# Kernel tuning notes

Hardware: AMD Instinct MI355X
Metric: run time of the kernel (lower is better)

## Reference

```python
import jax, jax.numpy as jnp
import numpy as np

T = 256          # tokens
H = 1024         # hidden_size
E = 64           # num_experts
I = 512          # routed intermediate_size
SI = 2048        # shared_expert_intermediate_size
TOP_K = 6
N_GROUP = 8
TOPK_GROUP = 4
ROUTED_SCALE = 2.5


def setup_inputs() -> dict:
    key = jax.random.key(0)
    ks = jax.random.split(key, 9)
    s = 0.02
    return {
        "hidden_states": jax.random.normal(ks[0], (T, H), jnp.float32),
        "gate_w": jax.random.normal(ks[1], (E, H), jnp.float32) * s,
        "e_bias": jax.random.normal(ks[2], (E,), jnp.float32) * 0.01,
        "w1": jax.random.normal(ks[3], (E, I, H), jnp.float32) * s,  # gate proj
        "w3": jax.random.normal(ks[4], (E, I, H), jnp.float32) * s,  # up proj
        "w2": jax.random.normal(ks[5], (E, H, I), jnp.float32) * s,  # down proj
        "ws_gate": jax.random.normal(ks[6], (SI, H), jnp.float32) * s,
        "ws_up": jax.random.normal(ks[7], (SI, H), jnp.float32) * s,
        "ws_down": jax.random.normal(ks[8], (H, SI), jnp.float32) * s,
    }


def _noaux_tc_routing(logits, e_bias):
    # DeepSeek-V3 group-limited sigmoid routing (is_thop=False path).
    scores = jax.nn.sigmoid(logits)                         # [T, E]
    swb = scores + e_bias                                   # bias only picks experts
    t, e = scores.shape
    g = swb.reshape(t, N_GROUP, e // N_GROUP)
    group_scores = jax.lax.top_k(g, 2)[0].sum(-1)           # top-2 sum per group [T, G]
    _, gidx = jax.lax.top_k(group_scores, TOPK_GROUP)
    gmask = jax.nn.one_hot(gidx, N_GROUP, dtype=scores.dtype).sum(-2)  # [T, G]
    smask = jnp.repeat(gmask, e // N_GROUP, axis=-1)        # [T, E]
    _, tidx = jax.lax.top_k(swb * smask, TOP_K)
    nmask = jax.nn.one_hot(tidx, e, dtype=scores.dtype).sum(-2)
    s = scores * nmask
    s = s / (s.sum(-1, keepdims=True) + 1e-20) * ROUTED_SCALE  # [T, E], TOP_K nonzeros
    # torch code returns topk(values, indices) of s; s itself is the dense
    # combine-weight matrix with exactly those values scattered at the indices.
    return s


def reference(hidden_states, gate_w, e_bias, w1, w3, w2, ws_gate, ws_up, ws_down):
    x = hidden_states
    # gate: cublas_mm with fp32 output
    logits = (x @ gate_w.T).astype(jnp.float32)             # [T, E]
    cw = _noaux_tc_routing(logits, e_bias)                  # [T, E] combine weights

    # routed experts: gated MLP per expert, combined by routing weights
    h1 = jnp.einsum('th,eih->tei', x, w1)
    h3 = jnp.einsum('th,eih->tei', x, w3)
    act = jax.nn.silu(h1) * h3                              # [T, E, I]
    eo = jnp.einsum('tei,ehi->teh', act, w2)                # [T, E, H]
    routed = jnp.einsum('teh,te->th', eo, cw.astype(x.dtype))

    # shared experts: GatedMLP
    shared = (jax.nn.silu(x @ ws_gate.T) * (x @ ws_up.T)) @ ws_down.T

    return shared + routed
```

## Files before the change

kernel.cpp:

```cpp
#include <hip/hip_runtime.h>
#include <math.h>

#define T_TOK 256
#define H_DIM 1024
#define E_NUM 64
#define I_DIM 512
#define SI_DIM 2048

#define BN 64
#define BM 32
#define BK 64
#define LDB 72

typedef __attribute__((ext_vector_type(8))) short short8;
typedef __attribute__((ext_vector_type(8))) __bf16 bf16x8;
typedef __attribute__((ext_vector_type(4))) float floatx4;
typedef __attribute__((ext_vector_type(4))) unsigned short ushort4v;

static __device__ __forceinline__ unsigned short f2bf(float f) {
  unsigned u = __float_as_uint(f);
  u += 0x7FFFu + ((u >> 16) & 1u);
  return (unsigned short)(u >> 16);
}

static __device__ __forceinline__ ushort4v pack4(floatx4 v) {
  ushort4v b;
  b[0] = f2bf(v[0]); b[1] = f2bf(v[1]); b[2] = f2bf(v[2]); b[3] = f2bf(v[3]);
  return b;
}

static __device__ __forceinline__ floatx4 mfma16(bf16x8 a, bf16x8 b, floatx4 c) {
  return __builtin_amdgcn_mfma_f32_16x16x32_bf16(a, b, c, 0, 0, 0);
}

__global__ __launch_bounds__(256) void gate_route_kernel(
    const float* __restrict__ x, const float* __restrict__ gw,
    const float* __restrict__ ebias, unsigned short* __restrict__ xbf,
    int* __restrict__ cnt, int* __restrict__ tok_list,
    float* __restrict__ wt_list) {
  const int t = blockIdx.x;
  const int j = threadIdx.x;
  __shared__ float xs[H_DIM];
  __shared__ double pd[4 * 64];

  floatx4 v = ((const floatx4*)(x + (size_t)t * H_DIM))[j];
  xs[4 * j + 0] = v[0]; xs[4 * j + 1] = v[1];
  xs[4 * j + 2] = v[2]; xs[4 * j + 3] = v[3];
  ((ushort4v*)(xbf + (size_t)t * H_DIM))[j] = pack4(v);
  __syncthreads();

  const int e = j & 63, ch = j >> 6;
  const float* wr = gw + (size_t)e * H_DIM + ch * 256;
  const float* xc = xs + ch * 256;
  double acc = 0.0;
  for (int i = 0; i < 64; ++i) {
    floatx4 w = ((const floatx4*)wr)[i];
    acc += (double)xc[4 * i + 0] * (double)w[0]
         + (double)xc[4 * i + 1] * (double)w[1]
         + (double)xc[4 * i + 2] * (double)w[2]
         + (double)xc[4 * i + 3] * (double)w[3];
  }
  pd[ch * 64 + e] = acc;
  __syncthreads();

  if (j < 64) {
    const int lane = j;
    const double logit = pd[lane] + pd[64 + lane] + pd[128 + lane] + pd[192 + lane];
    const double score = 1.0 / (1.0 + exp(-logit));
    const double swb = score + (double)ebias[lane];

    double m1 = swb, m2 = -1.0e300;
    #pragma unroll
    for (int d = 1; d < 8; d <<= 1) {
      double o1 = __shfl_xor(m1, d);
      double o2 = __shfl_xor(m2, d);
      double hi = fmax(m1, o1), lo = fmin(m1, o1);
      m1 = hi;
      m2 = fmax(lo, fmax(m2, o2));
    }
    const double gscore = m1 + m2;

    double gs[8];
    #pragma unroll
    for (int g = 0; g < 8; ++g) gs[g] = __shfl(gscore, g << 3);
    unsigned gsel = 0;
    #pragma unroll
    for (int it = 0; it < 4; ++it) {
      int best = 0; double bv = -1.0e300;
      #pragma unroll
      for (int g = 0; g < 8; ++g) {
        bool taken = (gsel >> g) & 1u;
        if (!taken && gs[g] > bv) { bv = gs[g]; best = g; }
      }
      gsel |= 1u << best;
    }

    double key = ((gsel >> (lane >> 3)) & 1u) ? swb : -1.0e300;
    int selected = 0;
    for (int it = 0; it < 6; ++it) {
      double vv = key; int idx = lane;
      #pragma unroll
      for (int d = 1; d < 64; d <<= 1) {
        double ov = __shfl_xor(vv, d);
        int oi = __shfl_xor(idx, d);
        if (ov > vv || (ov == vv && oi < idx)) { vv = ov; idx = oi; }
      }
      if (lane == idx) { selected = 1; key = -1.0e300; }
    }

    double ssum = selected ? score : 0.0;
    #pragma unroll
    for (int d = 1; d < 64; d <<= 1) ssum += __shfl_xor(ssum, d);

    if (selected) {
      float wgt = (float)(score / (ssum + 1e-20) * 2.5);
      int p = atomicAdd(&cnt[lane], 1);
      tok_list[lane * T_TOK + p] = t;
      wt_list[lane * T_TOK + p] = wgt;
    }
  }
}

__global__ __launch_bounds__(256, 2) void routed_gu_kernel(
    const unsigned short* __restrict__ xbf, const float* __restrict__ w1,
    const float* __restrict__ w3, const int* __restrict__ cnt,
    const int* __restrict__ tok_list, unsigned short* __restrict__ act_r) {
  __shared__ unsigned short sBg[BN * LDB];
  __shared__ unsigned short sBu[BN * LDB];
  __shared__ unsigned short sA[BM * LDB];
  __shared__ int stok[BM];

  const int e = blockIdx.x >> 3;
  const int n0 = (blockIdx.x & 7) * BN;
  const int j = threadIdx.x;
  const int wv = j >> 6, lane = j & 63;
  const int q = lane >> 4, c = lane & 15;
  const int ne = cnt[e];
  const int* tl = tok_list + e * T_TOK;
  unsigned short* ap = act_r + (size_t)e * T_TOK * I_DIM;
  const float* wgB = w1 + ((size_t)e * I_DIM + n0) * H_DIM;
  const float* wuB = w3 + ((size_t)e * I_DIM + n0) * H_DIM;

  const int wrow = j >> 4;
  const int wcol = (j & 15) * 4;
  const int arow = j >> 3;
  const int acol = (j & 7) * 8;

  for (int m0 = 0; m0 < ne; m0 += BM) {
    __syncthreads();
    if (j < BM) {
      int r = m0 + j;
      stok[j] = (r < ne) ? tl[r] : 0;
    }
    __syncthreads();
    const unsigned short* aRow = xbf + (size_t)stok[arow] * H_DIM;

    floatx4 pg[4], pu[4];
    bf16x8 pa;
    #pragma unroll
    for (int p = 0; p < 4; ++p) {
      pg[p] = *(const floatx4*)(wgB + (size_t)(p * 16 + wrow) * H_DIM + wcol);
      pu[p] = *(const floatx4*)(wuB + (size_t)(p * 16 + wrow) * H_DIM + wcol);
    }
    pa = *(const bf16x8*)(aRow + acol);

    floatx4 ag0 = (floatx4)0.0f, ag1 = (floatx4)0.0f;
    floatx4 au0 = (floatx4)0.0f, au1 = (floatx4)0.0f;
    for (int k0 = 0; k0 < H_DIM; k0 += BK) {
      if (k0) __syncthreads();
      #pragma unroll
      for (int p = 0; p < 4; ++p) {
        *(ushort4v*)(sBg + (p * 16 + wrow) * LDB + wcol) = pack4(pg[p]);
        *(ushort4v*)(sBu + (p * 16 + wrow) * LDB + wcol) = pack4(pu[p]);
      }
      *(bf16x8*)(sA + arow * LDB + acol) = pa;
      __syncthreads();
      if (k0 + BK < H_DIM) {
        const int kn = k0 + BK;
        #pragma unroll
        for (int p = 0; p < 4; ++p) {
          pg[p] = *(const floatx4*)(wgB + (size_t)(p * 16 + wrow) * H_DIM + kn + wcol);
          pu[p] = *(const floatx4*)(wuB + (size_t)(p * 16 + wrow) * H_DIM + kn + wcol);
        }
        pa = *(const bf16x8*)(aRow + kn + acol);
      }
      #pragma unroll
      for (int kk = 0; kk < BK; kk += 32) {
        const int ko = kk + q * 8;
        bf16x8 bg = *(const bf16x8*)(sBg + (wv * 16 + c) * LDB + ko);
        bf16x8 bu = *(const bf16x8*)(sBu + (wv * 16 + c) * LDB + ko);
        bf16x8 a0 = *(const bf16x8*)(sA + c * LDB + ko);
        bf16x8 a1 = *(const bf16x8*)(sA + (16 + c) * LDB + ko);
        ag0 = mfma16(a0, bg, ag0);
        ag1 = mfma16(a1, bg, ag1);
        au0 = mfma16(a0, bu, au0);
        au1 = mfma16(a1, bu, au1);
      }
    }
    #pragma unroll
    for (int s = 0; s < 2; ++s) {
      floatx4 g = s ? ag1 : ag0;
      floatx4 u = s ? au1 : au0;
      #pragma unroll
      for (int r = 0; r < 4; ++r) {
        const int m = m0 + s * 16 + q * 4 + r;
        if (m < ne) {
          float gg = g[r], uu = u[r];
          float a = gg / (1.0f + __expf(-gg)) * uu;
          ap[(size_t)m * I_DIM + n0 + wv * 16 + c] = f2bf(a);
        }
      }
    }
  }
}

__global__ __launch_bounds__(256, 2) void shared_gu_kernel(
    const unsigned short* __restrict__ xbf, const float* __restrict__ wsg,
    const float* __restrict__ wsu, unsigned short* __restrict__ act_s) {
  __shared__ unsigned short sBg[BN * LDB];
  __shared__ unsigned short sBu[BN * LDB];
  __shared__ unsigned short sA[BM * LDB];

  const int n0 = (blockIdx.x & 31) * BN;
  const int m0 = (blockIdx.x >> 5) * BM;
  const int j = threadIdx.x;
  const int wv = j >> 6, lane = j & 63;
  const int q = lane >> 4, c = lane & 15;
  const float* wgB = wsg + (size_t)n0 * H_DIM;
  const float* wuB = wsu + (size_t)n0 * H_DIM;

  const int wrow = j >> 4, wcol = (j & 15) * 4;
  const int arow = j >> 3, acol = (j & 7) * 8;
  const unsigned short* aRow = xbf + (size_t)(m0 + arow) * H_DIM;

  floatx4 pg[4], pu[4];
  bf16x8 pa;
  #pragma unroll
  for (int p = 0; p < 4; ++p) {
    pg[p] = *(const floatx4*)(wgB + (size_t)(p * 16 + wrow) * H_DIM + wcol);
    pu[p] = *(const floatx4*)(wuB + (size_t)(p * 16 + wrow) * H_DIM + wcol);
  }
  pa = *(const bf16x8*)(aRow + acol);

  floatx4 ag0 = (floatx4)0.0f, ag1 = (floatx4)0.0f;
  floatx4 au0 = (floatx4)0.0f, au1 = (floatx4)0.0f;
  for (int k0 = 0; k0 < H_DIM; k0 += BK) {
    if (k0) __syncthreads();
    #pragma unroll
    for (int p = 0; p < 4; ++p) {
      *(ushort4v*)(sBg + (p * 16 + wrow) * LDB + wcol) = pack4(pg[p]);
      *(ushort4v*)(sBu + (p * 16 + wrow) * LDB + wcol) = pack4(pu[p]);
    }
    *(bf16x8*)(sA + arow * LDB + acol) = pa;
    __syncthreads();
    if (k0 + BK < H_DIM) {
      const int kn = k0 + BK;
      #pragma unroll
      for (int p = 0; p < 4; ++p) {
        pg[p] = *(const floatx4*)(wgB + (size_t)(p * 16 + wrow) * H_DIM + kn + wcol);
        pu[p] = *(const floatx4*)(wuB + (size_t)(p * 16 + wrow) * H_DIM + kn + wcol);
      }
      pa = *(const bf16x8*)(aRow + kn + acol);
    }
    #pragma unroll
    for (int kk = 0; kk < BK; kk += 32) {
      const int ko = kk + q * 8;
      bf16x8 bg = *(const bf16x8*)(sBg + (wv * 16 + c) * LDB + ko);
      bf16x8 bu = *(const bf16x8*)(sBu + (wv * 16 + c) * LDB + ko);
      bf16x8 a0 = *(const bf16x8*)(sA + c * LDB + ko);
      bf16x8 a1 = *(const bf16x8*)(sA + (16 + c) * LDB + ko);
      ag0 = mfma16(a0, bg, ag0);
      ag1 = mfma16(a1, bg, ag1);
      au0 = mfma16(a0, bu, au0);
      au1 = mfma16(a1, bu, au1);
    }
  }
  #pragma unroll
  for (int s = 0; s < 2; ++s) {
    floatx4 g = s ? ag1 : ag0;
    floatx4 u = s ? au1 : au0;
    #pragma unroll
    for (int r = 0; r < 4; ++r) {
      const int m = m0 + s * 16 + q * 4 + r;
      float gg = g[r], uu = u[r];
      float a = gg / (1.0f + __expf(-gg)) * uu;
      act_s[(size_t)m * SI_DIM + n0 + wv * 16 + c] = f2bf(a);
    }
  }
}

__global__ __launch_bounds__(256, 2) void shared_down_kernel(
    const unsigned short* __restrict__ act_s, const float* __restrict__ wsd,
    float* __restrict__ out) {
  __shared__ unsigned short sB[BN * LDB];
  __shared__ unsigned short sA[BM * LDB];

  const int n0 = (blockIdx.x & 15) * BN;
  const int m0 = ((blockIdx.x >> 4) & 7) * BM;
  const int kh = blockIdx.x >> 7;
  const int kbeg = kh * (SI_DIM / 2);
  const int j = threadIdx.x;
  const int wv = j >> 6, lane = j & 63;
  const int q = lane >> 4, c = lane & 15;
  const float* wB = wsd + (size_t)n0 * SI_DIM;

  const int wrow = j >> 4, wcol = (j & 15) * 4;
  const int arow = j >> 3, acol = (j & 7) * 8;
  const unsigned short* aRow = act_s + (size_t)(m0 + arow) * SI_DIM;

  floatx4 pw[4];
  bf16x8 pa;
  #pragma unroll
  for (int p = 0; p < 4; ++p) {
    pw[p] = *(const floatx4*)(wB + (size_t)(p * 16 + wrow) * SI_DIM + kbeg + wcol);
  }
  pa = *(const bf16x8*)(aRow + kbeg + acol);

  floatx4 ac0 = (floatx4)0.0f, ac1 = (floatx4)0.0f;
  for (int kr = 0; kr < SI_DIM / 2; kr += BK) {
    const int k0 = kbeg + kr;
    if (kr) __syncthreads();
    #pragma unroll
    for (int p = 0; p < 4; ++p) {
      *(ushort4v*)(sB + (p * 16 + wrow) * LDB + wcol) = pack4(pw[p]);
    }
    *(bf16x8*)(sA + arow * LDB + acol) = pa;
    __syncthreads();
    if (kr + BK < SI_DIM / 2) {
      const int kn = k0 + BK;
      #pragma unroll
      for (int p = 0; p < 4; ++p) {
        pw[p] = *(const floatx4*)(wB + (size_t)(p * 16 + wrow) * SI_DIM + kn + wcol);
      }
      pa = *(const bf16x8*)(aRow + kn + acol);
    }
    #pragma unroll
    for (int kk = 0; kk < BK; kk += 32) {
      const int ko = kk + q * 8;
      bf16x8 b = *(const bf16x8*)(sB + (wv * 16 + c) * LDB + ko);
      bf16x8 a0 = *(const bf16x8*)(sA + c * LDB + ko);
      bf16x8 a1 = *(const bf16x8*)(sA + (16 + c) * LDB + ko);
      ac0 = mfma16(a0, b, ac0);
      ac1 = mfma16(a1, b, ac1);
    }
  }
  #pragma unroll
  for (int s = 0; s < 2; ++s) {
    floatx4 d = s ? ac1 : ac0;
    #pragma unroll
    for (int r = 0; r < 4; ++r) {
      const int m = m0 + s * 16 + q * 4 + r;
      atomicAdd(&out[(size_t)m * H_DIM + n0 + wv * 16 + c], d[r]);
    }
  }
}

__global__ __launch_bounds__(256, 2) void routed_down_kernel(
    const unsigned short* __restrict__ act_r, const float* __restrict__ w2,
    const int* __restrict__ cnt, const int* __restrict__ tok_list,
    const float* __restrict__ wt_list, float* __restrict__ out) {
  __shared__ unsigned short sB[BN * LDB];
  __shared__ unsigned short sA[BM * LDB];
  __shared__ int stok[BM];
  __shared__ float swl[BM];

  const int e = blockIdx.x >> 4;
  const int n0 = (blockIdx.x & 15) * BN;
  const int j = threadIdx.x;
  const int wv = j >> 6, lane = j & 63;
  const int q = lane >> 4, c = lane & 15;
  const int ne = cnt[e];
  const int* tl = tok_list + e * T_TOK;
  const float* wl = wt_list + e * T_TOK;
  const unsigned short* apb = act_r + (size_t)e * T_TOK * I_DIM;
  const float* wB = w2 + ((size_t)e * H_DIM + n0) * I_DIM;

  const int wrow = j >> 4, wcol = (j & 15) * 4;
  const int arow = j >> 3, acol = (j & 7) * 8;

  for (int m0 = 0; m0 < ne; m0 += BM) {
    __syncthreads();
    if (j < BM) {
      int r = m0 + j;
      bool ok = r < ne;
      stok[j] = ok ? tl[r] : 0;
      swl[j] = ok ? wl[r] : 0.0f;
    }
    int ar = m0 + arow;
    if (ar >= T_TOK) ar = T_TOK - 1;
    const unsigned short* aRow = apb + (size_t)ar * I_DIM;

    floatx4 pw[4];
    bf16x8 pa;
    #pragma unroll
    for (int p = 0; p < 4; ++p) {
      pw[p] = *(const floatx4*)(wB + (size_t)(p * 16 + wrow) * I_DIM + wcol);
    }
    pa = *(const bf16x8*)(aRow + acol);

    floatx4 ac0 = (floatx4)0.0f, ac1 = (floatx4)0.0f;
    for (int k0 = 0; k0 < I_DIM; k0 += BK) {
      __syncthreads();
      #pragma unroll
      for (int p = 0; p < 4; ++p) {
        *(ushort4v*)(sB + (p * 16 + wrow) * LDB + wcol) = pack4(pw[p]);
      }
      *(bf16x8*)(sA + arow * LDB + acol) = pa;
      __syncthreads();
      if (k0 + BK < I_DIM) {
        const int kn = k0 + BK;
        #pragma unroll
        for (int p = 0; p < 4; ++p) {
          pw[p] = *(const floatx4*)(wB + (size_t)(p * 16 + wrow) * I_DIM + kn + wcol);
        }
        pa = *(const bf16x8*)(aRow + kn + acol);
      }
      #pragma unroll
      for (int kk = 0; kk < BK; kk += 32) {
        const int ko = kk + q * 8;
        bf16x8 b = *(const bf16x8*)(sB + (wv * 16 + c) * LDB + ko);
        bf16x8 a0 = *(const bf16x8*)(sA + c * LDB + ko);
        bf16x8 a1 = *(const bf16x8*)(sA + (16 + c) * LDB + ko);
        ac0 = mfma16(a0, b, ac0);
        ac1 = mfma16(a1, b, ac1);
      }
    }
    #pragma unroll
    for (int s = 0; s < 2; ++s) {
      floatx4 d = s ? ac1 : ac0;
      #pragma unroll
      for (int r = 0; r < 4; ++r) {
        const int mi = s * 16 + q * 4 + r;
        if (m0 + mi < ne) {
          atomicAdd(&out[(size_t)stok[mi] * H_DIM + n0 + wv * 16 + c],
                    d[r] * swl[mi]);
        }
      }
    }
  }
}

extern "C" void kernel_launch(void* const* d_in, const int* in_sizes, int n_in,
                              void* d_out, int out_size, void* d_ws, size_t ws_size,
                              hipStream_t stream) {
  const float* x   = (const float*)d_in[0];
  const float* gw  = (const float*)d_in[1];
  const float* eb  = (const float*)d_in[2];
  const float* w1  = (const float*)d_in[3];
  const float* w3  = (const float*)d_in[4];
  const float* w2  = (const float*)d_in[5];
  const float* wsg = (const float*)d_in[6];
  const float* wsu = (const float*)d_in[7];
  const float* wsd = (const float*)d_in[8];
  float* out = (float*)d_out;

  char* ws = (char*)d_ws;
  unsigned short* xbf   = (unsigned short*)(ws);
  unsigned short* act_s = (unsigned short*)(ws + 524288);
  int*   cnt            = (int*)(ws + 1572864);
  int*   tok            = (int*)(ws + 1573120);
  float* wt             = (float*)(ws + 1638656);
  unsigned short* act_r = (unsigned short*)(ws + 1704192);

  hipMemsetAsync(cnt, 0, E_NUM * sizeof(int), stream);
  hipMemsetAsync(out, 0, (size_t)T_TOK * H_DIM * sizeof(float), stream);
  gate_route_kernel<<<dim3(T_TOK), dim3(256), 0, stream>>>(x, gw, eb, xbf, cnt, tok, wt);
  routed_gu_kernel<<<dim3(E_NUM * (I_DIM / BN)), dim3(256), 0, stream>>>(xbf, w1, w3, cnt, tok, act_r);
  shared_gu_kernel<<<dim3((SI_DIM / BN) * (T_TOK / BM)), dim3(256), 0, stream>>>(xbf, wsg, wsu, act_s);
  shared_down_kernel<<<dim3((H_DIM / BN) * (T_TOK / BM) * 2), dim3(256), 0, stream>>>(act_s, wsd, out);
  routed_down_kernel<<<dim3(E_NUM * (H_DIM / BN)), dim3(256), 0, stream>>>(act_r, w2, cnt, tok, wt, out);
}
```

Measured before the change: 469.8 us.

## Load fp32 weights directly into MFMA operand registers, stage only activations in LDS

The four GEMM kernels stop staging the fp32 weight tiles through shared memory. Each lane now reads its own weight row straight from global memory, converts it to bf16 in registers and feeds it to the MFMA as the B operand, with a one-step register prefetch. Only the activation rows go to LDS, staged in large 512-wide chunks with an XOR swizzle to avoid bank conflicts, which cuts the number of barriers per K loop. The cost is less coalesced global weight loads, each lane striding across rows, and less latency hiding, since only one step is prefetched and there is no LDS double buffering.

```diff
diff --git a/kernel.cpp b/kernel.cpp
--- a/kernel.cpp
+++ b/kernel.cpp
@@ -9,13 +9,12 @@
 
 #define BN 64
 #define BM 32
-#define BK 64
-#define LDB 72
 
 typedef __attribute__((ext_vector_type(8))) short short8;
 typedef __attribute__((ext_vector_type(8))) __bf16 bf16x8;
 typedef __attribute__((ext_vector_type(4))) float floatx4;
 typedef __attribute__((ext_vector_type(4))) unsigned short ushort4v;
+typedef __attribute__((ext_vector_type(8))) unsigned short ushort8;
 
 static __device__ __forceinline__ unsigned short f2bf(float f) {
   unsigned u = __float_as_uint(f);
@@ -27,6 +26,14 @@
   ushort4v b;
   b[0] = f2bf(v[0]); b[1] = f2bf(v[1]); b[2] = f2bf(v[2]); b[3] = f2bf(v[3]);
   return b;
+}
+
+static __device__ __forceinline__ bf16x8 pack8(floatx4 a, floatx4 b) {
+  ushort8 s;
+  s[0] = f2bf(a[0]); s[1] = f2bf(a[1]); s[2] = f2bf(a[2]); s[3] = f2bf(a[3]);
+  s[4] = f2bf(b[0]); s[5] = f2bf(b[1]); s[6] = f2bf(b[2]); s[7] = f2bf(b[3]);
+  union { ushort8 u; bf16x8 v; } cv; cv.u = s;
+  return cv.v;
 }
 
 static __device__ __forceinline__ floatx4 mfma16(bf16x8 a, bf16x8 b, floatx4 c) {
@@ -125,72 +132,61 @@
     const unsigned short* __restrict__ xbf, const float* __restrict__ w1,
     const float* __restrict__ w3, const int* __restrict__ cnt,
     const int* __restrict__ tok_list, unsigned short* __restrict__ act_r) {
-  __shared__ unsigned short sBg[BN * LDB];
-  __shared__ unsigned short sBu[BN * LDB];
-  __shared__ unsigned short sA[BM * LDB];
-  __shared__ int stok[BM];
+  __shared__ __align__(16) char sAB[BM * 1024];
 
   const int e = blockIdx.x >> 3;
   const int n0 = (blockIdx.x & 7) * BN;
   const int j = threadIdx.x;
   const int wv = j >> 6, lane = j & 63;
   const int q = lane >> 4, c = lane & 15;
+  const int kq = q * 8;
   const int ne = cnt[e];
+  if (ne <= 0) return;
   const int* tl = tok_list + e * T_TOK;
   unsigned short* ap = act_r + (size_t)e * T_TOK * I_DIM;
-  const float* wgB = w1 + ((size_t)e * I_DIM + n0) * H_DIM;
-  const float* wuB = w3 + ((size_t)e * I_DIM + n0) * H_DIM;
-
-  const int wrow = j >> 4;
-  const int wcol = (j & 15) * 4;
-  const int arow = j >> 3;
-  const int acol = (j & 7) * 8;
+
+  const float* wgR = w1 + ((size_t)e * I_DIM + n0 + wv * 16 + c) * H_DIM;
+  const float* wuR = w3 + ((size_t)e * I_DIM + n0 + wv * 16 + c) * H_DIM;
+
+  const int sr = j >> 3, st8 = (j & 7) * 8;
+  const int xrs = (sr & 7) << 4;
+  const int xr0 = (c & 7) << 4;
 
   for (int m0 = 0; m0 < ne; m0 += BM) {
-    __syncthreads();
-    if (j < BM) {
-      int r = m0 + j;
-      stok[j] = (r < ne) ? tl[r] : 0;
-    }
-    __syncthreads();
-    const unsigned short* aRow = xbf + (size_t)stok[arow] * H_DIM;
-
-    floatx4 pg[4], pu[4];
-    bf16x8 pa;
-    #pragma unroll
-    for (int p = 0; p < 4; ++p) {
-      pg[p] = *(const floatx4*)(wgB + (size_t)(p * 16 + wrow) * H_DIM + wcol);
-      pu[p] = *(const floatx4*)(wuB + (size_t)(p * 16 + wrow) * H_DIM + wcol);
-    }
-    pa = *(const bf16x8*)(aRow + acol);
+    const int tok = (m0 + sr < ne) ? tl[m0 + sr] : tl[m0];
+    const unsigned short* aRow = xbf + (size_t)tok * H_DIM;
+
+    floatx4 cg0 = *(const floatx4*)(wgR + kq);
+    floatx4 cg1 = *(const floatx4*)(wgR + kq + 4);
+    floatx4 cu0 = *(const floatx4*)(wuR + kq);
+    floatx4 cu1 = *(const floatx4*)(wuR + kq + 4);
 
     floatx4 ag0 = (floatx4)0.0f, ag1 = (floatx4)0.0f;
     floatx4 au0 = (floatx4)0.0f, au1 = (floatx4)0.0f;
-    for (int k0 = 0; k0 < H_DIM; k0 += BK) {
-      if (k0) __syncthreads();
-      #pragma unroll
-      for (int p = 0; p < 4; ++p) {
-        *(ushort4v*)(sBg + (p * 16 + wrow) * LDB + wcol) = pack4(pg[p]);
-        *(ushort4v*)(sBu + (p * 16 + wrow) * LDB + wcol) = pack4(pu[p]);
-      }
-      *(bf16x8*)(sA + arow * LDB + acol) = pa;
+
+    for (int half = 0; half < 2; ++half) {
+      const int kbase = half * 512;
       __syncthreads();
-      if (k0 + BK < H_DIM) {
-        const int kn = k0 + BK;
-        #pragma unroll
-        for (int p = 0; p < 4; ++p) {
-          pg[p] = *(const floatx4*)(wgB + (size_t)(p * 16 + wrow) * H_DIM + kn + wcol);
-          pu[p] = *(const floatx4*)(wuB + (size_t)(p * 16 + wrow) * H_DIM + kn + wcol);
+      #pragma unroll
+      for (int i = 0; i < 512; i += 64) {
+        const int col = st8 + i;
+        *(bf16x8*)(sAB + sr * 1024 + ((2 * col) ^ xrs)) =
+            *(const bf16x8*)(aRow + kbase + col);
+      }
+      __syncthreads();
+      for (int kcl = 0; kcl < 512; kcl += 32) {
+        const int kc = kbase + kcl;
+        bf16x8 bg = pack8(cg0, cg1);
+        bf16x8 bu = pack8(cu0, cu1);
+        if (kc + 32 < H_DIM) {
+          cg0 = *(const floatx4*)(wgR + kc + 32 + kq);
+          cg1 = *(const floatx4*)(wgR + kc + 32 + kq + 4);
+          cu0 = *(const floatx4*)(wuR + kc + 32 + kq);
+          cu1 = *(const floatx4*)(wuR + kc + 32 + kq + 4);
         }
-        pa = *(const bf16x8*)(aRow + kn + acol);
-      }
-      #pragma unroll
-      for (int kk = 0; kk < BK; kk += 32) {
-        const int ko = kk + q * 8;
-        bf16x8 bg = *(const bf16x8*)(sBg + (wv * 16 + c) * LDB + ko);
-        bf16x8 bu = *(const bf16x8*)(sBu + (wv * 16 + c) * LDB + ko);
-        bf16x8 a0 = *(const bf16x8*)(sA + c * LDB + ko);
-        bf16x8 a1 = *(const bf16x8*)(sA + (16 + c) * LDB + ko);
+        const int kb = 2 * (kcl + kq);
+        bf16x8 a0 = *(const bf16x8*)(sAB + c * 1024 + (kb ^ xr0));
+        bf16x8 a1 = *(const bf16x8*)(sAB + (16 + c) * 1024 + (kb ^ xr0));
         ag0 = mfma16(a0, bg, ag0);
         ag1 = mfma16(a1, bg, ag1);
         au0 = mfma16(a0, bu, au0);
@@ -217,58 +213,54 @@
 __global__ __launch_bounds__(256, 2) void shared_gu_kernel(
     const unsigned short* __restrict__ xbf, const float* __restrict__ wsg,
     const float* __restrict__ wsu, unsigned short* __restrict__ act_s) {
-  __shared__ unsigned short sBg[BN * LDB];
-  __shared__ unsigned short sBu[BN * LDB];
-  __shared__ unsigned short sA[BM * LDB];
+  __shared__ __align__(16) char sAB[BM * 1024];
 
   const int n0 = (blockIdx.x & 31) * BN;
   const int m0 = (blockIdx.x >> 5) * BM;
   const int j = threadIdx.x;
   const int wv = j >> 6, lane = j & 63;
   const int q = lane >> 4, c = lane & 15;
-  const float* wgB = wsg + (size_t)n0 * H_DIM;
-  const float* wuB = wsu + (size_t)n0 * H_DIM;
-
-  const int wrow = j >> 4, wcol = (j & 15) * 4;
-  const int arow = j >> 3, acol = (j & 7) * 8;
-  const unsigned short* aRow = xbf + (size_t)(m0 + arow) * H_DIM;
-
-  floatx4 pg[4], pu[4];
-  bf16x8 pa;
-  #pragma unroll
-  for (int p = 0; p < 4; ++p) {
-    pg[p] = *(const floatx4*)(wgB + (size_t)(p * 16 + wrow) * H_DIM + wcol);
-    pu[p] = *(const floatx4*)(wuB + (size_t)(p * 16 + wrow) * H_DIM + wcol);
-  }
-  pa = *(const bf16x8*)(aRow + acol);
+  const int kq = q * 8;
+
+  const float* wgR = wsg + (size_t)(n0 + wv * 16 + c) * H_DIM;
+  const float* wuR = wsu + (size_t)(n0 + wv * 16 + c) * H_DIM;
+
+  const int sr = j >> 3, st8 = (j & 7) * 8;
+  const int xrs = (sr & 7) << 4;
+  const int xr0 = (c & 7) << 4;
+  const unsigned short* aRow = xbf + (size_t)(m0 + sr) * H_DIM;
+
+  floatx4 cg0 = *(const floatx4*)(wgR + kq);
+  floatx4 cg1 = *(const floatx4*)(wgR + kq + 4);
+  floatx4 cu0 = *(const floatx4*)(wuR + kq);
+  floatx4 cu1 = *(const floatx4*)(wuR + kq + 4);
 
   floatx4 ag0 = (floatx4)0.0f, ag1 = (floatx4)0.0f;
   floatx4 au0 = (floatx4)0.0f, au1 = (floatx4)0.0f;
-  for (int k0 = 0; k0 < H_DIM; k0 += BK) {
-    if (k0) __syncthreads();
-    #pragma unroll
-    for (int p = 0; p < 4; ++p) {
-      *(ushort4v*)(sBg + (p * 16 + wrow) * LDB + wcol) = pack4(pg[p]);
-      *(ushort4v*)(sBu + (p * 16 + wrow) * LDB + wcol) = pack4(pu[p]);
-    }
-    *(bf16x8*)(sA + arow * LDB + acol) = pa;
-    __syncthreads();
-    if (k0 + BK < H_DIM) {
-      const int kn = k0 + BK;
-      #pragma unroll
-      for (int p = 0; p < 4; ++p) {
-        pg[p] = *(const floatx4*)(wgB + (size_t)(p * 16 + wrow) * H_DIM + kn + wcol);
-        pu[p] = *(const floatx4*)(wuB + (size_t)(p * 16 + wrow) * H_DIM + kn + wcol);
-      }
-      pa = *(const bf16x8*)(aRow + kn + acol);
-    }
-    #pragma unroll
-    for (int kk = 0; kk < BK; kk += 32) {
-      const int ko = kk + q * 8;
-      bf16x8 bg = *(const bf16x8*)(sBg + (wv * 16 + c) * LDB + ko);
-      bf16x8 bu = *(const bf16x8*)(sBu + (wv * 16 + c) * LDB + ko);
-      bf16x8 a0 = *(const bf16x8*)(sA + c * LDB + ko);
-      bf16x8 a1 = *(const bf16x8*)(sA + (16 + c) * LDB + ko);
+
+  for (int half = 0; half < 2; ++half) {
+    const int kbase = half * 512;
+    __syncthreads();
+    #pragma unroll
+    for (int i = 0; i < 512; i += 64) {
+      const int col = st8 + i;
+      *(bf16x8*)(sAB + sr * 1024 + ((2 * col) ^ xrs)) =
+          *(const bf16x8*)(aRow + kbase + col);
+    }
+    __syncthreads();
+    for (int kcl = 0; kcl < 512; kcl += 32) {
+      const int kc = kbase + kcl;
+      bf16x8 bg = pack8(cg0, cg1);
+      bf16x8 bu = pack8(cu0, cu1);
+      if (kc + 32 < H_DIM) {
+        cg0 = *(const floatx4*)(wgR + kc + 32 + kq);
+        cg1 = *(const floatx4*)(wgR + kc + 32 + kq + 4);
+        cu0 = *(const floatx4*)(wuR + kc + 32 + kq);
+        cu1 = *(const floatx4*)(wuR + kc + 32 + kq + 4);
+      }
+      const int kb = 2 * (kcl + kq);
+      bf16x8 a0 = *(const bf16x8*)(sAB + c * 1024 + (kb ^ xr0));
+      bf16x8 a1 = *(const bf16x8*)(sAB + (16 + c) * 1024 + (kb ^ xr0));
       ag0 = mfma16(a0, bg, ag0);
       ag1 = mfma16(a1, bg, ag1);
       au0 = mfma16(a0, bu, au0);
@@ -292,8 +284,7 @@
 __global__ __launch_bounds__(256, 2) void shared_down_kernel(
     const unsigned short* __restrict__ act_s, const float* __restrict__ wsd,
     float* __restrict__ out) {
-  __shared__ unsigned short sB[BN * LDB];
-  __shared__ unsigned short sA[BM * LDB];
+  __shared__ __align__(16) char sAB[BM * 1024];
 
   const int n0 = (blockIdx.x & 15) * BN;
   const int m0 = ((blockIdx.x >> 4) & 7) * BM;
@@ -302,44 +293,39 @@
   const int j = threadIdx.x;
   const int wv = j >> 6, lane = j & 63;
   const int q = lane >> 4, c = lane & 15;
-  const float* wB = wsd + (size_t)n0 * SI_DIM;
-
-  const int wrow = j >> 4, wcol = (j & 15) * 4;
-  const int arow = j >> 3, acol = (j & 7) * 8;
-  const unsigned short* aRow = act_s + (size_t)(m0 + arow) * SI_DIM;
-
-  floatx4 pw[4];
-  bf16x8 pa;
-  #pragma unroll
-  for (int p = 0; p < 4; ++p) {
-    pw[p] = *(const floatx4*)(wB + (size_t)(p * 16 + wrow) * SI_DIM + kbeg + wcol);
-  }
-  pa = *(const bf16x8*)(aRow + kbeg + acol);
+  const int kq = q * 8;
+
+  const float* wR = wsd + (size_t)(n0 + wv * 16 + c) * SI_DIM + kbeg;
+
+  const int sr = j >> 3, st8 = (j & 7) * 8;
+  const int xrs = (sr & 7) << 4;
+  const int xr0 = (c & 7) << 4;
+  const unsigned short* aRow = act_s + (size_t)(m0 + sr) * SI_DIM + kbeg;
+
+  floatx4 cw0 = *(const floatx4*)(wR + kq);
+  floatx4 cw1 = *(const floatx4*)(wR + kq + 4);
 
   floatx4 ac0 = (floatx4)0.0f, ac1 = (floatx4)0.0f;
-  for (int kr = 0; kr < SI_DIM / 2; kr += BK) {
-    const int k0 = kbeg + kr;
-    if (kr) __syncthreads();
-    #pragma unroll
-    for (int p = 0; p < 4; ++p) {
-      *(ushort4v*)(sB + (p * 16 + wrow) * LDB + wcol) = pack4(pw[p]);
-    }
-    *(bf16x8*)(sA + arow * LDB + acol) = pa;
-    __syncthreads();
-    if (kr + BK < SI_DIM / 2) {
-      const int kn = k0 + BK;
-      #pragma unroll
-      for (int p = 0; p < 4; ++p) {
-        pw[p] = *(const floatx4*)(wB + (size_t)(p * 16 + wrow) * SI_DIM + kn + wcol);
-      }
-      pa = *(const bf16x8*)(aRow + kn + acol);
-    }
-    #pragma unroll
-    for (int kk = 0; kk < BK; kk += 32) {
-      const int ko = kk + q * 8;
-      bf16x8 b = *(const bf16x8*)(sB + (wv * 16 + c) * LDB + ko);
-      bf16x8 a0 = *(const bf16x8*)(sA + c * LDB + ko);
-      bf16x8 a1 = *(const bf16x8*)(sA + (16 + c) * LDB + ko);
+  for (int half = 0; half < 2; ++half) {
+    const int kbase = half * 512;
+    __syncthreads();
+    #pragma unroll
+    for (int i = 0; i < 512; i += 64) {
+      const int col = st8 + i;
+      *(bf16x8*)(sAB + sr * 1024 + ((2 * col) ^ xrs)) =
+          *(const bf16x8*)(aRow + kbase + col);
+    }
+    __syncthreads();
+    for (int kcl = 0; kcl < 512; kcl += 32) {
+      const int kc = kbase + kcl;
+      bf16x8 b = pack8(cw0, cw1);
+      if (kc + 32 < SI_DIM / 2) {
+        cw0 = *(const floatx4*)(wR + kc + 32 + kq);
+        cw1 = *(const floatx4*)(wR + kc + 32 + kq + 4);
+      }
+      const int kb = 2 * (kcl + kq);
+      bf16x8 a0 = *(const bf16x8*)(sAB + c * 1024 + (kb ^ xr0));
+      bf16x8 a1 = *(const bf16x8*)(sAB + (16 + c) * 1024 + (kb ^ xr0));
       ac0 = mfma16(a0, b, ac0);
       ac1 = mfma16(a1, b, ac1);
     }
@@ -359,71 +345,55 @@
     const unsigned short* __restrict__ act_r, const float* __restrict__ w2,
     const int* __restrict__ cnt, const int* __restrict__ tok_list,
     const float* __restrict__ wt_list, float* __restrict__ out) {
-  __shared__ unsigned short sB[BN * LDB];
-  __shared__ unsigned short sA[BM * LDB];
-  __shared__ int stok[BM];
-  __shared__ float swl[BM];
+  __shared__ __align__(16) char sAB[BM * 1024];
 
   const int e = blockIdx.x >> 4;
   const int n0 = (blockIdx.x & 15) * BN;
   const int j = threadIdx.x;
   const int wv = j >> 6, lane = j & 63;
   const int q = lane >> 4, c = lane & 15;
+  const int kq = q * 8;
   const int ne = cnt[e];
+  if (ne <= 0) return;
   const int* tl = tok_list + e * T_TOK;
   const float* wl = wt_list + e * T_TOK;
   const unsigned short* apb = act_r + (size_t)e * T_TOK * I_DIM;
-  const float* wB = w2 + ((size_t)e * H_DIM + n0) * I_DIM;
-
-  const int wrow = j >> 4, wcol = (j & 15) * 4;
-  const int arow = j >> 3, acol = (j & 7) * 8;
+  const float* wR = w2 + ((size_t)e * H_DIM + n0 + wv * 16 + c) * I_DIM;
+
+  const int sr = j >> 3, st8 = (j & 7) * 8;
+  const int xrs = (sr & 7) << 4;
+  const int xr0 = (c & 7) << 4;
 
   for (int m0 = 0; m0 < ne; m0 += BM) {
     __syncthreads();
-    if (j < BM) {
-      int r = m0 + j;
-      bool ok = r < ne;
-      stok[j] = ok ? tl[r] : 0;
-      swl[j] = ok ? wl[r] : 0.0f;
-    }
-    int ar = m0 + arow;
-    if (ar >= T_TOK) ar = T_TOK - 1;
-    const unsigned short* aRow = apb + (size_t)ar * I_DIM;
-
-    floatx4 pw[4];
-    bf16x8 pa;
-    #pragma unroll
-    for (int p = 0; p < 4; ++p) {
-      pw[p] = *(const floatx4*)(wB + (size_t)(p * 16 + wrow) * I_DIM + wcol);
-    }
-    pa = *(const bf16x8*)(aRow + acol);
+    {
+      int ar = m0 + sr;
+      if (ar >= ne) ar = m0;
+      const unsigned short* aRow = apb + (size_t)ar * I_DIM;
+      #pragma unroll
+      for (int i = 0; i < I_DIM; i += 64) {
+        const int col = st8 + i;
+        *(bf16x8*)(sAB + sr * 1024 + ((2 * col) ^ xrs)) =
+            *(const bf16x8*)(aRow + col);
+      }
+    }
+    __syncthreads();
+
+    floatx4 cw0 = *(const floatx4*)(wR + kq);
+    floatx4 cw1 = *(const floatx4*)(wR + kq + 4);
 
     floatx4 ac0 = (floatx4)0.0f, ac1 = (floatx4)0.0f;
-    for (int k0 = 0; k0 < I_DIM; k0 += BK) {
-      __syncthreads();
-      #pragma unroll
-      for (int p = 0; p < 4; ++p) {
-        *(ushort4v*)(sB + (p * 16 + wrow) * LDB + wcol) = pack4(pw[p]);
-      }
-      *(bf16x8*)(sA + arow * LDB + acol) = pa;
-      __syncthreads();
-      if (k0 + BK < I_DIM) {
-        const int kn = k0 + BK;
-        #pragma unroll
-        for (int p = 0; p < 4; ++p) {
-          pw[p] = *(const floatx4*)(wB + (size_t)(p * 16 + wrow) * I_DIM + kn + wcol);
-        }
-        pa = *(const bf16x8*)(aRow + kn + acol);
-      }
-      #pragma unroll
-      for (int kk = 0; kk < BK; kk += 32) {
-        const int ko = kk + q * 8;
-        bf16x8 b = *(const bf16x8*)(sB + (wv * 16 + c) * LDB + ko);
-        bf16x8 a0 = *(const bf16x8*)(sA + c * LDB + ko);
-        bf16x8 a1 = *(const bf16x8*)(sA + (16 + c) * LDB + ko);
-        ac0 = mfma16(a0, b, ac0);
-        ac1 = mfma16(a1, b, ac1);
-      }
+    for (int kc = 0; kc < I_DIM; kc += 32) {
+      bf16x8 b = pack8(cw0, cw1);
+      if (kc + 32 < I_DIM) {
+        cw0 = *(const floatx4*)(wR + kc + 32 + kq);
+        cw1 = *(const floatx4*)(wR + kc + 32 + kq + 4);
+      }
+      const int kb = 2 * (kc + kq);
+      bf16x8 a0 = *(const bf16x8*)(sAB + c * 1024 + (kb ^ xr0));
+      bf16x8 a1 = *(const bf16x8*)(sAB + (16 + c) * 1024 + (kb ^ xr0));
+      ac0 = mfma16(a0, b, ac0);
+      ac1 = mfma16(a1, b, ac1);
     }
     #pragma unroll
     for (int s = 0; s < 2; ++s) {
@@ -432,8 +402,8 @@
       for (int r = 0; r < 4; ++r) {
         const int mi = s * 16 + q * 4 + r;
         if (m0 + mi < ne) {
-          atomicAdd(&out[(size_t)stok[mi] * H_DIM + n0 + wv * 16 + c],
-                    d[r] * swl[mi]);
+          atomicAdd(&out[(size_t)tl[m0 + mi] * H_DIM + n0 + wv * 16 + c],
+                    d[r] * wl[m0 + mi]);
         }
       }
     }
```

New measurement: 480.6 us. 1.02x slower.
